# Performance work log

Measured on AMD Instinct MI355X. Metric: run time of the kernel, lower is better.

Reference implementation:

```python
import jax, jax.numpy as jnp
import numpy as np

EPS = 1e-5


def _create_scalars(x0, x, N, basis, v):
    # x0: [b,NT,3], x/v: [b,NT,ND,3], N: [b,NT], basis: [b,Nb,3]
    b, NT, ND, _ = x.shape
    v0 = jnp.mean(v, axis=2)                       # [b,NT,3]
    v = v - v0[:, :, None, :]
    feats = []
    # local_N normalization (log scaling)
    Nn = jnp.log1p(N.astype(x.dtype))
    feats.append(jnp.broadcast_to(Nn[:, :, None, None], (b, NT, ND, 1)))
    x0n = jnp.linalg.norm(x0, axis=-1, keepdims=True) + EPS   # [b,NT,1]
    feats.append(jnp.broadcast_to(x0n[:, :, None, :], (b, NT, ND, 1)))
    x0u = x0 / x0n
    x0b = jnp.einsum('bid,bjd->bij', x0u, basis)              # [b,NT,Nb]
    feats.append(jnp.broadcast_to(x0b[:, :, None, :], (b, NT, ND, x0b.shape[-1])))
    v0n = jnp.linalg.norm(v0, axis=-1, keepdims=True) + EPS
    feats.append(jnp.broadcast_to(v0n[:, :, None, :], (b, NT, ND, 1)))
    v0u = v0 / v0n
    v0b = jnp.einsum('bid,bjd->bij', v0u, basis)
    feats.append(jnp.broadcast_to(v0b[:, :, None, :], (b, NT, ND, v0b.shape[-1])))
    x0v0 = jnp.einsum('bid,bid->bi', x0u, v0u)                # [b,NT]
    feats.append(jnp.broadcast_to(x0v0[:, :, None, None], (b, NT, ND, 1)))
    xn = jnp.linalg.norm(x, axis=-1, keepdims=True) + EPS     # [b,NT,ND,1]
    feats.append(xn)
    xu = x / xn
    feats.append(jnp.einsum('bijd,bkd->bijk', xu, basis))     # [b,NT,ND,Nb]
    vn = jnp.linalg.norm(v, axis=-1, keepdims=True) + EPS
    feats.append(vn)
    vu = v / vn
    feats.append(jnp.einsum('bijd,bkd->bijk', vu, basis))
    feats.append(jnp.einsum('bijd,bijd->bij', xu, vu)[..., None])
    return jnp.concatenate(feats, axis=-1)                    # [b,NT,ND,19]


def setup_inputs() -> dict:
    key = jax.random.key(0)
    ks = jax.random.split(key, 12)
    b, NT, ND, Nb = 4, 1024, 128, 3
    k_in, H, L = 19, 256, 128
    s0 = 1.0 / np.sqrt(k_in)
    s1 = 1.0 / np.sqrt(H)
    return {
        'x0': jax.random.normal(ks[0], (b, NT, 3), jnp.float32),
        'x': jax.random.normal(ks[1], (b, NT, ND, 3), jnp.float32),
        'N': jax.random.randint(ks[2], (b, NT), 1, 1000),
        'basis': jax.random.normal(ks[3], (b, Nb, 3), jnp.float32),
        'v': jax.random.normal(ks[4], (b, NT, ND, 3), jnp.float32),
        'W0': jax.random.normal(ks[5], (k_in, H), jnp.float32) * s0,
        'b0': jnp.zeros((H,), jnp.float32),
        'W1': jax.random.normal(ks[6], (H, H), jnp.float32) * s1,
        'b1': jnp.zeros((H,), jnp.float32),
        'W2': jax.random.normal(ks[7], (H, L), jnp.float32) * s1,
        'b2': jnp.zeros((L,), jnp.float32),
    }


def reference(x0, x, N, basis, v, W0, b0, W1, b1, W2, b2):
    s = _create_scalars(x0, x, N, basis, v)            # [b,NT,ND,19]
    h = jax.nn.leaky_relu(s @ W0 + b0)                 # layer 0 MLP
    h = jnp.mean(h, axis=2)                            # pool over N_DM -> [b,NT,H]
    h = jax.nn.leaky_relu(h @ W1 + b1)                 # layer 1
    return h @ W2 + b2                                 # layer 2 -> [b,NT,Nlatent]
```

## Files before the change

### kernel.cpp

```cpp
#include <hip/hip_runtime.h>
#include <math.h>

#define EPSF 1e-5f
constexpr int NT  = 1024;
constexpr int ND  = 128;
constexpr int KIN = 19;
constexpr int H   = 256;
constexpr int L   = 128;

typedef __attribute__((ext_vector_type(8))) short short8;
typedef __attribute__((ext_vector_type(4))) float f32x4;

static __device__ inline unsigned cvt_pk_bf16(float lo, float hi) {
    unsigned r;
    asm("v_cvt_pk_bf16_f32 %0, %1, %2" : "=v"(r) : "v"(lo), "v"(hi));
    return r;
}

__global__ __launch_bounds__(256) void k_feat_l0(
    const float* __restrict__ x0, const float* __restrict__ x,
    const int*   __restrict__ Nv, const float* __restrict__ basis,
    const float* __restrict__ v,  const float* __restrict__ W0,
    const float* __restrict__ b0, float* __restrict__ hm_out)
{
    const int tid  = threadIdx.x;
    const int lane = tid & 63;
    const int w    = tid >> 6;
    const int g    = blockIdx.x;
    const int bidx = g >> 10;

    __shared__ __align__(16) ushort featb[512 * 8];

    if (w < 2) {
        const float* xp = x + (size_t)g * (ND * 3);
        const float* vp = v + (size_t)g * (ND * 3);
        float V0[3], V1[3], X[3];
        #pragma unroll
        for (int j = 0; j < 3; ++j) {
            V0[j] = vp[lane*3 + j];
            V1[j] = vp[(lane + 64)*3 + j];
            X[j]  = xp[(w*64 + lane)*3 + j];
        }

        float sx = V0[0] + V1[0];
        float sy = V0[1] + V1[1];
        float sz = V0[2] + V1[2];
        #pragma unroll
        for (int m = 1; m < 64; m <<= 1) {
            sx += __shfl_xor(sx, m, 64);
            sy += __shfl_xor(sy, m, 64);
            sz += __shfl_xor(sz, m, 64);
        }
        const float invd = 1.0f / (float)ND;
        const float v0x = sx * invd, v0y = sy * invd, v0z = sz * invd;

        const float* bs = basis + bidx * 9;
        float fs[10];
        {
            const float ax = x0[g*3+0], ay = x0[g*3+1], az = x0[g*3+2];
            const float x0n = sqrtf(ax*ax + ay*ay + az*az) + EPSF;
            const float v0n = sqrtf(v0x*v0x + v0y*v0y + v0z*v0z) + EPSF;
            const float ix  = 1.f / x0n, iv0 = 1.f / v0n;
            fs[0] = log1pf((float)Nv[g]);
            fs[1] = x0n;
            fs[2] = (ax*bs[0] + ay*bs[1] + az*bs[2]) * ix;
            fs[3] = (ax*bs[3] + ay*bs[4] + az*bs[5]) * ix;
            fs[4] = (ax*bs[6] + ay*bs[7] + az*bs[8]) * ix;
            fs[5] = v0n;
            fs[6] = (v0x*bs[0] + v0y*bs[1] + v0z*bs[2]) * iv0;
            fs[7] = (v0x*bs[3] + v0y*bs[4] + v0z*bs[5]) * iv0;
            fs[8] = (v0x*bs[6] + v0y*bs[7] + v0z*bs[8]) * iv0;
            fs[9] = (ax*v0x + ay*v0y + az*v0z) * ix * iv0;
        }

        const float vx = (w == 0) ? V0[0] : V1[0];
        const float vy = (w == 0) ? V0[1] : V1[1];
        const float vz = (w == 0) ? V0[2] : V1[2];
        const float cx = vx - v0x, cy = vy - v0y, cz = vz - v0z;
        const float xx = X[0], xy = X[1], xz = X[2];
        const float xn = sqrtf(xx*xx + xy*xy + xz*xz) + EPSF;
        const float vn = sqrtf(cx*cx + cy*cy + cz*cz) + EPSF;
        const float ixn = 1.f/xn, ivn = 1.f/vn;
        float f[20];
        #pragma unroll
        for (int k = 0; k < 10; ++k) f[k] = fs[k];
        f[10] = xn;
        f[11] = (xx*bs[0] + xy*bs[1] + xz*bs[2]) * ixn;
        f[12] = (xx*bs[3] + xy*bs[4] + xz*bs[5]) * ixn;
        f[13] = (xx*bs[6] + xy*bs[7] + xz*bs[8]) * ixn;
        f[14] = vn;
        f[15] = (cx*bs[0] + cy*bs[1] + cz*bs[2]) * ivn;
        f[16] = (cx*bs[3] + cy*bs[4] + cz*bs[5]) * ivn;
        f[17] = (cx*bs[6] + cy*bs[7] + cz*bs[8]) * ivn;
        f[18] = (xx*cx + xy*cy + xz*cz) * ixn * ivn;
        f[19] = 1.0f;

        const int mt  = w * 4 + (lane >> 4);
        const int r16 = lane & 15;
        uint4* base = reinterpret_cast<uint4*>(&featb[((mt << 6) + r16) * 8]);
        uint4 pk0, pk1, pk2;
        pk0.x = cvt_pk_bf16(f[0],  f[1]);  pk0.y = cvt_pk_bf16(f[2],  f[3]);
        pk0.z = cvt_pk_bf16(f[4],  f[5]);  pk0.w = cvt_pk_bf16(f[6],  f[7]);
        pk1.x = cvt_pk_bf16(f[8],  f[9]);  pk1.y = cvt_pk_bf16(f[10], f[11]);
        pk1.z = cvt_pk_bf16(f[12], f[13]); pk1.w = cvt_pk_bf16(f[14], f[15]);
        pk2.x = cvt_pk_bf16(f[16], f[17]); pk2.y = cvt_pk_bf16(f[18], f[19]);
        pk2.z = 0u; pk2.w = 0u;
        base[0]  = pk0;
        base[16] = pk1;
        base[32] = pk2;
        base[48] = uint4{0u,0u,0u,0u};
    }
    __syncthreads();

    short8 bfrag[4];
    {
        const int col16 = lane & 15;
        const int kb    = lane >> 4;
        #pragma unroll
        for (int nt = 0; nt < 4; ++nt) {
            const int col = w * 64 + nt * 16 + col16;
            float fv[8];
            #pragma unroll
            for (int j = 0; j < 8; ++j) {
                const int k = kb * 8 + j;
                fv[j] = (k < KIN) ? W0[k * H + col] : ((k == KIN) ? b0[col] : 0.f);
            }
            uint4 pk;
            pk.x = cvt_pk_bf16(fv[0], fv[1]);
            pk.y = cvt_pk_bf16(fv[2], fv[3]);
            pk.z = cvt_pk_bf16(fv[4], fv[5]);
            pk.w = cvt_pk_bf16(fv[6], fv[7]);
            bfrag[nt] = *reinterpret_cast<short8*>(&pk);
        }
    }

    const f32x4 zc = {0.f, 0.f, 0.f, 0.f};
    f32x4 psum[4];
    #pragma unroll
    for (int nt = 0; nt < 4; ++nt)
        #pragma unroll
        for (int r = 0; r < 4; ++r) psum[nt][r] = 0.f;

    #pragma unroll 2
    for (int mt = 0; mt < 8; ++mt) {
        const short8 af = *reinterpret_cast<const short8*>(
            &featb[((mt << 6) + lane) * 8]);
        #pragma unroll
        for (int nt = 0; nt < 4; ++nt) {
            f32x4 d = __builtin_amdgcn_mfma_f32_16x16x32_bf16(af, bfrag[nt], zc, 0, 0, 0);
            #pragma unroll
            for (int r = 0; r < 4; ++r) {
                const float a = d[r];
                psum[nt][r] = fmaf(0.505f, a, fmaf(0.495f, fabsf(a), psum[nt][r]));
            }
        }
    }

    const float invd = 1.0f / (float)ND;
    #pragma unroll
    for (int nt = 0; nt < 4; ++nt) {
        float s4 = psum[nt][0] + psum[nt][1] + psum[nt][2] + psum[nt][3];
        s4 += __shfl_xor(s4, 16, 64);
        s4 += __shfl_xor(s4, 32, 64);
        if (lane < 16)
            hm_out[(size_t)g * H + w * 64 + nt * 16 + lane] = s4 * invd;
    }
}

__global__ __launch_bounds__(256) void k_l12(
    const float* __restrict__ hm, const float* __restrict__ W1,
    const float* __restrict__ b1, const float* __restrict__ W2,
    const float* __restrict__ b2, float* __restrict__ out)
{
    const int tb  = blockIdx.x * 8;
    const int tid = threadIdx.x;
    __shared__ float hs[8][H];
    __shared__ float h1[8][H];

    {
        const float4* src = reinterpret_cast<const float4*>(hm + (size_t)tb * H);
        float4* dst = reinterpret_cast<float4*>(&hs[0][0]);
        #pragma unroll
        for (int i = 0; i < 2; ++i) dst[tid + i*256] = src[tid + i*256];
    }
    __syncthreads();

    {
        float acc[8];
        const float bb = b1[tid];
        #pragma unroll
        for (int t = 0; t < 8; ++t) acc[t] = bb;
        for (int k = 0; k < H; ++k) {
            const float w = W1[(size_t)k * H + tid];
            #pragma unroll
            for (int t = 0; t < 8; ++t) acc[t] = fmaf(hs[t][k], w, acc[t]);
        }
        #pragma unroll
        for (int t = 0; t < 8; ++t) {
            float a = acc[t];
            h1[t][tid] = (a > 0.f) ? a : 0.01f * a;
        }
    }
    __syncthreads();

    {
        const int n  = tid & 127;
        const int t0 = (tid >> 7) * 4;
        float acc[4];
        const float bb = b2[n];
        #pragma unroll
        for (int t = 0; t < 4; ++t) acc[t] = bb;
        for (int k = 0; k < H; ++k) {
            const float w = W2[(size_t)k * L + n];
            #pragma unroll
            for (int t = 0; t < 4; ++t) acc[t] = fmaf(h1[t0 + t][k], w, acc[t]);
        }
        #pragma unroll
        for (int t = 0; t < 4; ++t)
            out[(size_t)(tb + t0 + t) * L + n] = acc[t];
    }
}

extern "C" void kernel_launch(void* const* d_in, const int* in_sizes, int n_in,
                              void* d_out, int out_size, void* d_ws, size_t ws_size,
                              hipStream_t stream) {
    const float* x0    = (const float*)d_in[0];
    const float* x     = (const float*)d_in[1];
    const int*   Nv    = (const int*)  d_in[2];
    const float* basis = (const float*)d_in[3];
    const float* v     = (const float*)d_in[4];
    const float* W0    = (const float*)d_in[5];
    const float* b0    = (const float*)d_in[6];
    const float* W1    = (const float*)d_in[7];
    const float* b1    = (const float*)d_in[8];
    const float* W2    = (const float*)d_in[9];
    const float* b2    = (const float*)d_in[10];
    float* out = (float*)d_out;
    float* hm  = (float*)d_ws;

    hipLaunchKernelGGL(k_feat_l0, dim3(4 * NT), dim3(256), 0, stream,
                       x0, x, Nv, basis, v, W0, b0, hm);
    hipLaunchKernelGGL(k_l12, dim3(4 * NT / 8), dim3(256), 0, stream,
                       hm, W1, b1, W2, b2, out);
}
```

Before: 49.46 us.

## Split fused feature+layer0 kernel into separate feature and MFMA kernels

The fused feature/layer-0 kernel is split in two. One kernel computes bf16 features for all 128 DM points of two groups per block, using every thread, and writes them to a global workspace in the MFMA fragment layout. A second kernel reads those fragments and runs the bf16 MFMA layer-0 with leaky-relu pooling, each wave handling two groups. This removes the idle waves in the feature phase and the block-wide barrier, but adds a global round trip for the features and an extra kernel launch.

```diff
diff --git a/kernel.cpp b/kernel.cpp
--- a/kernel.cpp
+++ b/kernel.cpp
@@ -17,100 +17,102 @@
     return r;
 }
 
-__global__ __launch_bounds__(256) void k_feat_l0(
+__global__ __launch_bounds__(256) void k_feat(
     const float* __restrict__ x0, const float* __restrict__ x,
     const int*   __restrict__ Nv, const float* __restrict__ basis,
-    const float* __restrict__ v,  const float* __restrict__ W0,
+    const float* __restrict__ v,  uint4* __restrict__ featw)
+{
+    const int tid  = threadIdx.x;
+    const int sub  = tid >> 7;
+    const int d    = tid & 127;
+    const int w    = tid >> 6;
+    const int lane = tid & 63;
+    const int g    = blockIdx.x * 2 + sub;
+    const int bidx = g >> 10;
+
+    __shared__ float wsum[4][3];
+
+    const float* xp = x + (size_t)g * (ND * 3);
+    const float* vp = v + (size_t)g * (ND * 3);
+    const float vx = vp[d*3+0], vy = vp[d*3+1], vz = vp[d*3+2];
+    const float xx = xp[d*3+0], xy = xp[d*3+1], xz = xp[d*3+2];
+
+    float sx = vx, sy = vy, sz = vz;
+    #pragma unroll
+    for (int m = 1; m < 64; m <<= 1) {
+        sx += __shfl_xor(sx, m, 64);
+        sy += __shfl_xor(sy, m, 64);
+        sz += __shfl_xor(sz, m, 64);
+    }
+    if (lane == 0) { wsum[w][0] = sx; wsum[w][1] = sy; wsum[w][2] = sz; }
+    __syncthreads();
+    const float invd = 1.0f / (float)ND;
+    const float v0x = (wsum[sub*2][0] + wsum[sub*2+1][0]) * invd;
+    const float v0y = (wsum[sub*2][1] + wsum[sub*2+1][1]) * invd;
+    const float v0z = (wsum[sub*2][2] + wsum[sub*2+1][2]) * invd;
+
+    const float* bs = basis + bidx * 9;
+    float fs[10];
+    {
+        const float ax = x0[g*3+0], ay = x0[g*3+1], az = x0[g*3+2];
+        const float x0n = sqrtf(ax*ax + ay*ay + az*az) + EPSF;
+        const float v0n = sqrtf(v0x*v0x + v0y*v0y + v0z*v0z) + EPSF;
+        const float ix  = 1.f / x0n, iv0 = 1.f / v0n;
+        fs[0] = log1pf((float)Nv[g]);
+        fs[1] = x0n;
+        fs[2] = (ax*bs[0] + ay*bs[1] + az*bs[2]) * ix;
+        fs[3] = (ax*bs[3] + ay*bs[4] + az*bs[5]) * ix;
+        fs[4] = (ax*bs[6] + ay*bs[7] + az*bs[8]) * ix;
+        fs[5] = v0n;
+        fs[6] = (v0x*bs[0] + v0y*bs[1] + v0z*bs[2]) * iv0;
+        fs[7] = (v0x*bs[3] + v0y*bs[4] + v0z*bs[5]) * iv0;
+        fs[8] = (v0x*bs[6] + v0y*bs[7] + v0z*bs[8]) * iv0;
+        fs[9] = (ax*v0x + ay*v0y + az*v0z) * ix * iv0;
+    }
+
+    const float cx = vx - v0x, cy = vy - v0y, cz = vz - v0z;
+    const float xn = sqrtf(xx*xx + xy*xy + xz*xz) + EPSF;
+    const float vn = sqrtf(cx*cx + cy*cy + cz*cz) + EPSF;
+    const float ixn = 1.f/xn, ivn = 1.f/vn;
+    float f[20];
+    #pragma unroll
+    for (int k = 0; k < 10; ++k) f[k] = fs[k];
+    f[10] = xn;
+    f[11] = (xx*bs[0] + xy*bs[1] + xz*bs[2]) * ixn;
+    f[12] = (xx*bs[3] + xy*bs[4] + xz*bs[5]) * ixn;
+    f[13] = (xx*bs[6] + xy*bs[7] + xz*bs[8]) * ixn;
+    f[14] = vn;
+    f[15] = (cx*bs[0] + cy*bs[1] + cz*bs[2]) * ivn;
+    f[16] = (cx*bs[3] + cy*bs[4] + cz*bs[5]) * ivn;
+    f[17] = (cx*bs[6] + cy*bs[7] + cz*bs[8]) * ivn;
+    f[18] = (xx*cx + xy*cy + xz*cz) * ixn * ivn;
+    f[19] = 1.0f;
+
+    uint4 pk0, pk1, pk2;
+    pk0.x = cvt_pk_bf16(f[0],  f[1]);  pk0.y = cvt_pk_bf16(f[2],  f[3]);
+    pk0.z = cvt_pk_bf16(f[4],  f[5]);  pk0.w = cvt_pk_bf16(f[6],  f[7]);
+    pk1.x = cvt_pk_bf16(f[8],  f[9]);  pk1.y = cvt_pk_bf16(f[10], f[11]);
+    pk1.z = cvt_pk_bf16(f[12], f[13]); pk1.w = cvt_pk_bf16(f[14], f[15]);
+    pk2.x = cvt_pk_bf16(f[16], f[17]); pk2.y = cvt_pk_bf16(f[18], f[19]);
+    pk2.z = 0u; pk2.w = 0u;
+
+    const int mt  = d >> 4;
+    const int r16 = d & 15;
+    uint4* base = featw + ((size_t)g * 384 + mt * 48 + r16);
+    base[0]  = pk0;
+    base[16] = pk1;
+    base[32] = pk2;
+}
+
+__global__ __launch_bounds__(256) void k_l0(
+    const uint4* __restrict__ featw, const float* __restrict__ W0,
     const float* __restrict__ b0, float* __restrict__ hm_out)
 {
-    const int tid  = threadIdx.x;
-    const int lane = tid & 63;
-    const int w    = tid >> 6;
-    const int g    = blockIdx.x;
-    const int bidx = g >> 10;
-
-    __shared__ __align__(16) ushort featb[512 * 8];
-
-    if (w < 2) {
-        const float* xp = x + (size_t)g * (ND * 3);
-        const float* vp = v + (size_t)g * (ND * 3);
-        float V0[3], V1[3], X[3];
-        #pragma unroll
-        for (int j = 0; j < 3; ++j) {
-            V0[j] = vp[lane*3 + j];
-            V1[j] = vp[(lane + 64)*3 + j];
-            X[j]  = xp[(w*64 + lane)*3 + j];
-        }
-
-        float sx = V0[0] + V1[0];
-        float sy = V0[1] + V1[1];
-        float sz = V0[2] + V1[2];
-        #pragma unroll
-        for (int m = 1; m < 64; m <<= 1) {
-            sx += __shfl_xor(sx, m, 64);
-            sy += __shfl_xor(sy, m, 64);
-            sz += __shfl_xor(sz, m, 64);
-        }
-        const float invd = 1.0f / (float)ND;
-        const float v0x = sx * invd, v0y = sy * invd, v0z = sz * invd;
-
-        const float* bs = basis + bidx * 9;
-        float fs[10];
-        {
-            const float ax = x0[g*3+0], ay = x0[g*3+1], az = x0[g*3+2];
-            const float x0n = sqrtf(ax*ax + ay*ay + az*az) + EPSF;
-            const float v0n = sqrtf(v0x*v0x + v0y*v0y + v0z*v0z) + EPSF;
-            const float ix  = 1.f / x0n, iv0 = 1.f / v0n;
-            fs[0] = log1pf((float)Nv[g]);
-            fs[1] = x0n;
-            fs[2] = (ax*bs[0] + ay*bs[1] + az*bs[2]) * ix;
-            fs[3] = (ax*bs[3] + ay*bs[4] + az*bs[5]) * ix;
-            fs[4] = (ax*bs[6] + ay*bs[7] + az*bs[8]) * ix;
-            fs[5] = v0n;
-            fs[6] = (v0x*bs[0] + v0y*bs[1] + v0z*bs[2]) * iv0;
-            fs[7] = (v0x*bs[3] + v0y*bs[4] + v0z*bs[5]) * iv0;
-            fs[8] = (v0x*bs[6] + v0y*bs[7] + v0z*bs[8]) * iv0;
-            fs[9] = (ax*v0x + ay*v0y + az*v0z) * ix * iv0;
-        }
-
-        const float vx = (w == 0) ? V0[0] : V1[0];
-        const float vy = (w == 0) ? V0[1] : V1[1];
-        const float vz = (w == 0) ? V0[2] : V1[2];
-        const float cx = vx - v0x, cy = vy - v0y, cz = vz - v0z;
-        const float xx = X[0], xy = X[1], xz = X[2];
-        const float xn = sqrtf(xx*xx + xy*xy + xz*xz) + EPSF;
-        const float vn = sqrtf(cx*cx + cy*cy + cz*cz) + EPSF;
-        const float ixn = 1.f/xn, ivn = 1.f/vn;
-        float f[20];
-        #pragma unroll
-        for (int k = 0; k < 10; ++k) f[k] = fs[k];
-        f[10] = xn;
-        f[11] = (xx*bs[0] + xy*bs[1] + xz*bs[2]) * ixn;
-        f[12] = (xx*bs[3] + xy*bs[4] + xz*bs[5]) * ixn;
-        f[13] = (xx*bs[6] + xy*bs[7] + xz*bs[8]) * ixn;
-        f[14] = vn;
-        f[15] = (cx*bs[0] + cy*bs[1] + cz*bs[2]) * ivn;
-        f[16] = (cx*bs[3] + cy*bs[4] + cz*bs[5]) * ivn;
-        f[17] = (cx*bs[6] + cy*bs[7] + cz*bs[8]) * ivn;
-        f[18] = (xx*cx + xy*cy + xz*cz) * ixn * ivn;
-        f[19] = 1.0f;
-
-        const int mt  = w * 4 + (lane >> 4);
-        const int r16 = lane & 15;
-        uint4* base = reinterpret_cast<uint4*>(&featb[((mt << 6) + r16) * 8]);
-        uint4 pk0, pk1, pk2;
-        pk0.x = cvt_pk_bf16(f[0],  f[1]);  pk0.y = cvt_pk_bf16(f[2],  f[3]);
-        pk0.z = cvt_pk_bf16(f[4],  f[5]);  pk0.w = cvt_pk_bf16(f[6],  f[7]);
-        pk1.x = cvt_pk_bf16(f[8],  f[9]);  pk1.y = cvt_pk_bf16(f[10], f[11]);
-        pk1.z = cvt_pk_bf16(f[12], f[13]); pk1.w = cvt_pk_bf16(f[14], f[15]);
-        pk2.x = cvt_pk_bf16(f[16], f[17]); pk2.y = cvt_pk_bf16(f[18], f[19]);
-        pk2.z = 0u; pk2.w = 0u;
-        base[0]  = pk0;
-        base[16] = pk1;
-        base[32] = pk2;
-        base[48] = uint4{0u,0u,0u,0u};
-    }
-    __syncthreads();
+    const int tid   = threadIdx.x;
+    const int lane  = tid & 63;
+    const int wid   = blockIdx.x * 4 + (tid >> 6);
+    const int cg    = wid & 3;
+    const int gbase = (wid >> 2) * 2;
 
     short8 bfrag[4];
     {
@@ -118,7 +120,7 @@
         const int kb    = lane >> 4;
         #pragma unroll
         for (int nt = 0; nt < 4; ++nt) {
-            const int col = w * 64 + nt * 16 + col16;
+            const int col = cg * 64 + nt * 16 + col16;
             float fv[8];
             #pragma unroll
             for (int j = 0; j < 8; ++j) {
@@ -135,35 +137,42 @@
     }
 
     const f32x4 zc = {0.f, 0.f, 0.f, 0.f};
-    f32x4 psum[4];
-    #pragma unroll
-    for (int nt = 0; nt < 4; ++nt)
-        #pragma unroll
-        for (int r = 0; r < 4; ++r) psum[nt][r] = 0.f;
-
-    #pragma unroll 2
-    for (int mt = 0; mt < 8; ++mt) {
-        const short8 af = *reinterpret_cast<const short8*>(
-            &featb[((mt << 6) + lane) * 8]);
+    const float invd = 1.0f / (float)ND;
+
+    #pragma unroll 1
+    for (int gi = 0; gi < 2; ++gi) {
+        const int g = gbase + gi;
+        f32x4 psum[4];
+        #pragma unroll
+        for (int nt = 0; nt < 4; ++nt)
+            #pragma unroll
+            for (int r = 0; r < 4; ++r) psum[nt][r] = 0.f;
+
+        #pragma unroll
+        for (int mt = 0; mt < 8; ++mt) {
+            uint4 a4 = {0u, 0u, 0u, 0u};
+            if (lane < 48)
+                a4 = featw[(size_t)g * 384 + mt * 48 + lane];
+            const short8 af = *reinterpret_cast<const short8*>(&a4);
+            #pragma unroll
+            for (int nt = 0; nt < 4; ++nt) {
+                f32x4 d = __builtin_amdgcn_mfma_f32_16x16x32_bf16(af, bfrag[nt], zc, 0, 0, 0);
+                #pragma unroll
+                for (int r = 0; r < 4; ++r) {
+                    const float a = d[r];
+                    psum[nt][r] = fmaf(0.505f, a, fmaf(0.495f, fabsf(a), psum[nt][r]));
+                }
+            }
+        }
+
         #pragma unroll
         for (int nt = 0; nt < 4; ++nt) {
-            f32x4 d = __builtin_amdgcn_mfma_f32_16x16x32_bf16(af, bfrag[nt], zc, 0, 0, 0);
-            #pragma unroll
-            for (int r = 0; r < 4; ++r) {
-                const float a = d[r];
-                psum[nt][r] = fmaf(0.505f, a, fmaf(0.495f, fabsf(a), psum[nt][r]));
-            }
-        }
-    }
-
-    const float invd = 1.0f / (float)ND;
-    #pragma unroll
-    for (int nt = 0; nt < 4; ++nt) {
-        float s4 = psum[nt][0] + psum[nt][1] + psum[nt][2] + psum[nt][3];
-        s4 += __shfl_xor(s4, 16, 64);
-        s4 += __shfl_xor(s4, 32, 64);
-        if (lane < 16)
-            hm_out[(size_t)g * H + w * 64 + nt * 16 + lane] = s4 * invd;
+            float s4 = psum[nt][0] + psum[nt][1] + psum[nt][2] + psum[nt][3];
+            s4 += __shfl_xor(s4, 16, 64);
+            s4 += __shfl_xor(s4, 32, 64);
+            if (lane < 16)
+                hm_out[(size_t)g * H + cg * 64 + nt * 16 + lane] = s4 * invd;
+        }
     }
 }
 
@@ -236,10 +245,14 @@
     const float* W2    = (const float*)d_in[9];
     const float* b2    = (const float*)d_in[10];
     float* out = (float*)d_out;
-    float* hm  = (float*)d_ws;
-
-    hipLaunchKernelGGL(k_feat_l0, dim3(4 * NT), dim3(256), 0, stream,
-                       x0, x, Nv, basis, v, W0, b0, hm);
+
+    float* hm   = (float*)d_ws;
+    uint4* feat = (uint4*)((char*)d_ws + (size_t)4*1024*1024);
+
+    hipLaunchKernelGGL(k_feat, dim3(4 * NT / 2), dim3(256), 0, stream,
+                       x0, x, Nv, basis, v, feat);
+    hipLaunchKernelGGL(k_l0, dim3(4 * NT / 2), dim3(256), 0, stream,
+                       feat, W0, b0, hm);
     hipLaunchKernelGGL(k_l12, dim3(4 * NT / 8), dim3(256), 0, stream,
                        hm, W1, b1, W2, b2, out);
 }
```

After: 76.24 us. 54.1% more time.
